# Optimization experiments

Measured on AMD Instinct MI355X. Metric: run time of the kernel, lower is better.

## Reference

```python
import jax, jax.numpy as jnp
import numpy as np

NUM_HEADS = 2
D = 512
D_HID = 2048


def _layer_norm(x, g, b, eps):
    mu = jnp.mean(x, axis=-1, keepdims=True)
    var = jnp.var(x, axis=-1, keepdims=True)
    return (x - mu) * jax.lax.rsqrt(var + eps) * g + b


def _attn_block(Q, K, V, resnet, Wq, Wk, Wv, ln_g, ln_b, w1, w2, fln_g, fln_b):
    # Linear projections (torch Linear: x @ W.T), no bias
    q = Q @ Wq.T
    k = K @ Wk.T
    v = V @ Wv.T
    B, N, C = q.shape
    gs = C // NUM_HEADS  # group size per head
    # split channels into heads == reshape [B,N,H,gs] -> [B,H,N,gs]
    qh = q.reshape(B, N, NUM_HEADS, gs).transpose(0, 2, 1, 3)
    kh = k.reshape(B, K.shape[1], NUM_HEADS, gs).transpose(0, 2, 1, 3)
    vh = v.reshape(B, V.shape[1], NUM_HEADS, gs).transpose(0, 2, 1, 3)
    scores = jnp.einsum('bhqd,bhkd->bhqk', qh, kh) / jnp.sqrt(jnp.asarray(gs, q.dtype))
    attn = jax.nn.softmax(scores, axis=-1)
    out = jnp.einsum('bhqk,bhkd->bhqd', attn, vh)
    # concat heads back to channel dim
    out = out.transpose(0, 2, 1, 3).reshape(B, N, C)
    x = out + resnet
    x = _layer_norm(x, ln_g, ln_b, 1e-5)
    # FFN (dropout is identity in eval mode)
    residual = x
    y = jax.nn.relu(x @ w1.T) @ w2.T
    y = y + residual
    y = _layer_norm(y, fln_g, fln_b, 1e-6)
    return y


def setup_inputs() -> dict:
    key = jax.random.key(0)
    ks = jax.random.split(key, 16)
    B, N = 4, 2048
    Fm = jax.random.normal(ks[0], (B, N, D), dtype=jnp.float32)
    Fs = jax.random.normal(ks[1], (B, N, D), dtype=jnp.float32)
    Fq = jax.random.normal(ks[2], (B, N, D), dtype=jnp.float32)
    s = 0.02
    Wq = jax.random.normal(ks[3], (3, D, D), dtype=jnp.float32) * s
    Wk = jax.random.normal(ks[4], (3, D, D), dtype=jnp.float32) * s
    Wv = jax.random.normal(ks[5], (3, D, D), dtype=jnp.float32) * s
    ln_g = jnp.ones((3, D), dtype=jnp.float32)
    ln_b = jnp.zeros((3, D), dtype=jnp.float32)
    w1 = jax.random.normal(ks[6], (3, D_HID, D), dtype=jnp.float32) * s
    w2 = jax.random.normal(ks[7], (3, D, D_HID), dtype=jnp.float32) * s
    fln_g = jnp.ones((3, D), dtype=jnp.float32)
    fln_b = jnp.zeros((3, D), dtype=jnp.float32)
    return {"Fm": Fm, "Fs": Fs, "Fq": Fq, "Wq": Wq, "Wk": Wk, "Wv": Wv,
            "ln_g": ln_g, "ln_b": ln_b, "w1": w1, "w2": w2,
            "fln_g": fln_g, "fln_b": fln_b, "out_dim": 512}


def reference(Fm, Fs, Fq, Wq, Wk, Wv, ln_g, ln_b, w1, w2, fln_g, fln_b, out_dim):
    def blk(i, Q, K, V, resnet):
        return _attn_block(Q, K, V, resnet, Wq[i], Wk[i], Wv[i], ln_g[i], ln_b[i],
                           w1[i], w2[i], fln_g[i], fln_b[i])
    css = blk(0, Fs, Fs, Fm, Fm)
    cqq = blk(1, Fq, Fq, Fq, Fq)
    csq = blk(2, cqq, Fs, css, css)
    return csq
```

## Files before the change

### kernel.cpp

```cpp
#include <hip/hip_runtime.h>

typedef __bf16 bf16_t;
typedef __bf16 bf16x8 __attribute__((ext_vector_type(8)));
typedef __bf16 bf16x4 __attribute__((ext_vector_type(4)));
typedef float  f32x4  __attribute__((ext_vector_type(4)));

#define GAS __attribute__((address_space(1)))
#define LAS __attribute__((address_space(3)))

enum { EPI_BF16 = 0, EPI_RELU = 1 };

struct GPtrs {
    const bf16_t* A[6];
    const bf16_t* B[6];
    bf16_t*       C[6];
};

__global__ void probe_dtype(const unsigned* __restrict__ lng_bits, int* __restrict__ flag)
{
    *flag = (lng_bits[0] == 0x3F800000u) ? 0 : 1;
}

__global__ __launch_bounds__(256) void conv_any3(
    const void* __restrict__ s0, const void* __restrict__ s1, const void* __restrict__ s2,
    bf16_t* __restrict__ d0, bf16_t* __restrict__ d1, bf16_t* __restrict__ d2,
    const int* __restrict__ flag, int n8)
{
    int i = blockIdx.x * 256 + threadIdx.x;
    if (i >= n8) return;
    const void* src = (blockIdx.z == 0) ? s0 : (blockIdx.z == 1) ? s1 : s2;
    bf16_t*    dst = (blockIdx.z == 0) ? d0 : (blockIdx.z == 1) ? d1 : d2;
    if (*flag == 0) {
        const float4* s = (const float4*)src;
        float4 a = s[i * 2], b = s[i * 2 + 1];
        bf16x8 o = { (bf16_t)a.x, (bf16_t)a.y, (bf16_t)a.z, (bf16_t)a.w,
                     (bf16_t)b.x, (bf16_t)b.y, (bf16_t)b.z, (bf16_t)b.w };
        ((bf16x8*)dst)[i] = o;
    } else {
        ((uint4*)dst)[i] = ((const uint4*)src)[i];
    }
}

__global__ __launch_bounds__(256) void widen_ln4(
    const void* __restrict__ a, const void* __restrict__ b,
    const void* __restrict__ c, const void* __restrict__ d,
    float* __restrict__ dst, const int* __restrict__ flag, int n)
{
    int i = blockIdx.x * 256 + threadIdx.x;
    int seg = i / n, j = i - seg * n;
    if (seg >= 4) return;
    const void* s = (seg == 0) ? a : (seg == 1) ? b : (seg == 2) ? c : d;
    dst[i] = (*flag == 0) ? ((const float*)s)[j]
                          : (float)((const bf16_t*)s)[j];
}

template<int EPI, int TMv, int TNv, bool TABLE, int ZH, bool VT>
__global__ __launch_bounds__(256) void gemm_bt(
    GPtrs P, int K, int lda, int ldb, int ldc,
    long sAb, long sAh, long sBb, long sBh, long sCb, long sCh,
    float scale)
{
    constexpr int MF = TMv / 32, NF = TNv / 32;
    constexpr int STG = 2 * (TMv + TNv) * 32;
    constexpr int RPK = TMv * TNv;
    constexpr int SME = (STG > RPK) ? STG : RPK;
    __shared__ __align__(16) bf16_t smem[SME];
    bf16_t* Asb = smem;
    bf16_t* Bsb = smem + 2 * TMv * 32;

    const int z = blockIdx.z;
    const bf16_t* A; const bf16_t* B; bf16_t* C; long cOff = 0;
    if constexpr (TABLE) {
        A = P.A[z]; B = P.B[z]; C = P.C[z];
    } else {
        const int half = z / ZH, zz = z % ZH;
        const long zb = zz >> 1, zh = zz & 1;
        A = P.A[half] + zb * sAb + zh * sAh;
        B = P.B[half] + zb * sBb + zh * sBh;
        C = P.C[half]; cOff = zb * sCb + zh * sCh;
    }

    int m_t, n_t;
    {
        const int gx = gridDim.x, gy = gridDim.y;
        if ((gy & 7) == 0) {
            const int L = blockIdx.y * gx + blockIdx.x;
            const int band_h = gy >> 3;
            const int r = L >> 3;
            m_t = (L & 7) * band_h + (r % band_h);
            n_t = r / band_h;
        } else { m_t = blockIdx.y; n_t = blockIdx.x; }
    }
    const int n0 = n_t * TNv;
    const int m0 = m_t * TMv;

    const int tid  = threadIdx.x;
    const int wave = tid >> 6, lane = tid & 63;
    const int wm = (wave >> 1) * (TMv / 2);
    const int wn = (wave & 1) * (TNv / 2);
    const int lrow = lane & 15, lquad = lane >> 4;
    const int rq   = (lquad ^ ((lrow >> 1) & 3)) * 8;
    const int drow = lane >> 2;
    const int dcol = (((lane & 3) ^ ((lane >> 3) & 3))) * 8;

    f32x4 acc[MF][NF];
    #pragma unroll
    for (int i = 0; i < MF; i++)
        #pragma unroll
        for (int j = 0; j < NF; j++) acc[i][j] = (f32x4){0.f, 0.f, 0.f, 0.f};

    const bf16_t* aP = A + (long)(m0 + wave * (TMv / 4) + drow) * lda + dcol;
    const bf16_t* bP = B + (long)(n0 + wave * (TNv / 4) + drow) * ldb + dcol;
    bf16_t* asW = Asb + wave * (TMv / 4) * 32;
    bf16_t* bsW = Bsb + wave * (TNv / 4) * 32;

    for (int kk = 0; kk < K; kk += 64) {
        __syncthreads();
        #pragma unroll
        for (int p = 0; p < 2; p++) {
            #pragma unroll
            for (int i = 0; i < TMv / 64; i++)
                __builtin_amdgcn_global_load_lds(
                    (GAS void*)(aP + p * 32 + (long)i * 16 * lda),
                    (LAS void*)(asW + p * TMv * 32 + i * 16 * 32), 16, 0, 0);
            #pragma unroll
            for (int i = 0; i < TNv / 64; i++)
                __builtin_amdgcn_global_load_lds(
                    (GAS void*)(bP + p * 32 + (long)i * 16 * ldb),
                    (LAS void*)(bsW + p * TNv * 32 + i * 16 * 32), 16, 0, 0);
        }
        aP += 64; bP += 64;
        __syncthreads();

        #pragma unroll
        for (int p = 0; p < 2; p++) {
            bf16x8 af[MF], bfr[NF];
            #pragma unroll
            for (int mi = 0; mi < MF; mi++)
                af[mi] = *(const bf16x8*)&Asb[(p * TMv + wm + mi * 16 + lrow) * 32 + rq];
            #pragma unroll
            for (int ni = 0; ni < NF; ni++)
                bfr[ni] = *(const bf16x8*)&Bsb[(p * TNv + wn + ni * 16 + lrow) * 32 + rq];
            #pragma unroll
            for (int mi = 0; mi < MF; mi++)
                #pragma unroll
                for (int ni = 0; ni < NF; ni++)
                    acc[mi][ni] = __builtin_amdgcn_mfma_f32_16x16x32_bf16(
                        af[mi], bfr[ni], acc[mi][ni], 0, 0, 0);
        }
    }

    if (VT && (z % 3 == 2)) {
        #pragma unroll
        for (int mi = 0; mi < MF; mi++)
            #pragma unroll
            for (int ni = 0; ni < NF; ni++) {
                const int mr = m0 + wm + mi * 16 + lquad * 4;
                const int nc = n0 + wn + ni * 16 + lrow;
                const int b = mr >> 11, s = mr & 2047;
                const int h = nc >> 8,  d = nc & 255;
                bf16x4 t = { (bf16_t)(acc[mi][ni][0]),
                             (bf16_t)(acc[mi][ni][1]),
                             (bf16_t)(acc[mi][ni][2]),
                             (bf16_t)(acc[mi][ni][3]) };
                *(bf16x4*)&C[(((long)(b * 2 + h) * 256 + d) << 11) + s] = t;
            }
        return;
    }

    __syncthreads();
    #pragma unroll
    for (int mi = 0; mi < MF; mi++)
        #pragma unroll
        for (int ni = 0; ni < NF; ni++)
            #pragma unroll
            for (int r = 0; r < 4; r++) {
                float v = acc[mi][ni][r] * scale;
                if (EPI == EPI_RELU) v = fmaxf(v, 0.f);
                smem[(wm + mi * 16 + lquad * 4 + r) * TNv + wn + ni * 16 + lrow] = (bf16_t)v;
            }
    __syncthreads();
    constexpr int TPR = TNv / 8;
    constexpr int RPP = 256 / TPR;
    const int srow = tid / TPR;
    const int scol = (tid % TPR) * 8;
    #pragma unroll
    for (int pass = 0; pass < TMv / RPP; pass++) {
        const int rr = pass * RPP + srow;
        bf16x8 vv = *(const bf16x8*)&smem[rr * TNv + scol];
        *(bf16x8*)&C[cOff + (long)(m0 + rr) * ldc + n0 + scol] = vv;
    }
}

__global__ __launch_bounds__(256) void softmax_rows(bf16_t* __restrict__ buf)
{
    const long base = (long)blockIdx.x * 2048;
    const int tid = threadIdx.x;
    const int wave = tid >> 6, lane = tid & 63;
    __shared__ float red[8];
    bf16x8 x = *(const bf16x8*)&buf[base + tid * 8];
    float v[8];
    float mx = -1e30f;
    #pragma unroll
    for (int j = 0; j < 8; j++) { v[j] = (float)x[j]; mx = fmaxf(mx, v[j]); }
    for (int off = 32; off; off >>= 1) mx = fmaxf(mx, __shfl_xor(mx, off));
    if (lane == 0) red[wave] = mx;
    __syncthreads();
    mx = fmaxf(fmaxf(red[0], red[1]), fmaxf(red[2], red[3]));
    float s = 0.f;
    #pragma unroll
    for (int j = 0; j < 8; j++) { v[j] = __expf(v[j] - mx); s += v[j]; }
    for (int off = 32; off; off >>= 1) s += __shfl_xor(s, off);
    if (lane == 0) red[4 + wave] = s;
    __syncthreads();
    s = red[4] + red[5] + red[6] + red[7];
    const float inv = 1.f / s;
    bf16x8 y;
    #pragma unroll
    for (int j = 0; j < 8; j++) y[j] = (bf16_t)(v[j] * inv);
    *(bf16x8*)&buf[base + tid * 8] = y;
}

__global__ __launch_bounds__(256) void add_ln2(
    const bf16_t* xA, const bf16_t* rA, const float* gA, const float* bA, bf16_t* oA,
    const bf16_t* xB, const bf16_t* rB, const float* gB, const float* bB, bf16_t* oB,
    float eps, int splitRows)
{
    const int wave = threadIdx.x >> 6, lane = threadIdx.x & 63;
    long row = (long)blockIdx.x * 4 + wave;
    const bf16_t* xin; const bf16_t* res; const float* g; const float* bias; bf16_t* out;
    if (row >= splitRows) {
        row -= splitRows;
        xin = xB; res = rB; g = gB; bias = bB; out = oB;
    } else {
        xin = xA; res = rA; g = gA; bias = bA; out = oA;
    }
    const long base = row * 512 + lane * 8;
    bf16x8 a8 = *(const bf16x8*)&xin[base];
    bf16x8 r8 = *(const bf16x8*)&res[base];
    float v[8];
    #pragma unroll
    for (int j = 0; j < 8; j++) v[j] = (float)a8[j] + (float)r8[j];
    float s = 0.f, s2 = 0.f;
    #pragma unroll
    for (int j = 0; j < 8; j++) { s += v[j]; s2 += v[j] * v[j]; }
    for (int off = 32; off; off >>= 1) { s += __shfl_xor(s, off); s2 += __shfl_xor(s2, off); }
    const float mu  = s * (1.f / 512.f);
    const float var = s2 * (1.f / 512.f) - mu * mu;
    const float rs  = rsqrtf(var + eps);
    const int c0 = lane * 8;
    float4 g0 = *(const float4*)&g[c0];
    float4 g1 = *(const float4*)&g[c0 + 4];
    float4 b0 = *(const float4*)&bias[c0];
    float4 b1 = *(const float4*)&bias[c0 + 4];
    float gv[8] = { g0.x, g0.y, g0.z, g0.w, g1.x, g1.y, g1.z, g1.w };
    float bv[8] = { b0.x, b0.y, b0.z, b0.w, b1.x, b1.y, b1.z, b1.w };
    #pragma unroll
    for (int j = 0; j < 8; j++)
        out[base + j] = (bf16_t)((v[j] - mu) * rs * gv[j] + bv[j]);
}

__global__ __launch_bounds__(256) void add_ln_f32(
    const bf16_t* xin, const bf16_t* __restrict__ res,
    const float* __restrict__ g, const float* __restrict__ bias,
    float* out, float eps)
{
    const int wave = threadIdx.x >> 6, lane = threadIdx.x & 63;
    const long row = (long)blockIdx.x * 4 + wave;
    const long base = row * 512 + lane * 8;
    bf16x8 a8 = *(const bf16x8*)&xin[base];
    bf16x8 r8 = *(const bf16x8*)&res[base];
    float v[8];
    #pragma unroll
    for (int j = 0; j < 8; j++) v[j] = (float)a8[j] + (float)r8[j];
    float s = 0.f, s2 = 0.f;
    #pragma unroll
    for (int j = 0; j < 8; j++) { s += v[j]; s2 += v[j] * v[j]; }
    for (int off = 32; off; off >>= 1) { s += __shfl_xor(s, off); s2 += __shfl_xor(s2, off); }
    const float mu  = s * (1.f / 512.f);
    const float var = s2 * (1.f / 512.f) - mu * mu;
    const float rs  = rsqrtf(var + eps);
    const int c0 = lane * 8;
    float4 g0 = *(const float4*)&g[c0];
    float4 g1 = *(const float4*)&g[c0 + 4];
    float4 b0 = *(const float4*)&bias[c0];
    float4 b1 = *(const float4*)&bias[c0 + 4];
    float gv[8] = { g0.x, g0.y, g0.z, g0.w, g1.x, g1.y, g1.z, g1.w };
    float bv[8] = { b0.x, b0.y, b0.z, b0.w, b1.x, b1.y, b1.z, b1.w };
    #pragma unroll
    for (int j = 0; j < 8; j++)
        out[base + j] = (v[j] - mu) * rs * gv[j] + bv[j];
}

extern "C" void kernel_launch(void* const* d_in, const int* in_sizes, int n_in,
                              void* d_out, int out_size, void* d_ws, size_t ws_size,
                              hipStream_t stream)
{
    const void* Fm    = d_in[0];
    const void* Fs    = d_in[1];
    const void* Fq    = d_in[2];
    const void* Wq    = d_in[3];
    const void* Wk    = d_in[4];
    const void* Wv    = d_in[5];
    const void* ln_g  = d_in[6];
    const void* ln_b  = d_in[7];
    const void* w1    = d_in[8];
    const void* w2    = d_in[9];
    const void* fln_g = d_in[10];
    const void* fln_b = d_in[11];
    (void)in_sizes; (void)n_in; (void)out_size; (void)ws_size;

    char* ws = (char*)d_ws;
    size_t off = 0;
    auto take = [&](size_t bytes) {
        char* p = ws + off;
        off += (bytes + 255) & ~(size_t)255;
        return p;
    };
    const size_t NT = 8192ul * 512;

    int*    flag = (int*)take(256);
    float*  lnw  = (float*)take(4ul * 1536 * 4);
    bf16_t* Fm_b = (bf16_t*)take(NT * 2);
    bf16_t* Fs_b = (bf16_t*)take(NT * 2);
    bf16_t* Fq_b = (bf16_t*)take(NT * 2);
    bf16_t* wqb  = (bf16_t*)take(3ul * 512 * 512 * 2);
    bf16_t* wkb  = (bf16_t*)take(3ul * 512 * 512 * 2);
    bf16_t* wvb  = (bf16_t*)take(3ul * 512 * 512 * 2);
    bf16_t* w1b  = (bf16_t*)take(3ul * 2048 * 512 * 2);
    bf16_t* w2b  = (bf16_t*)take(3ul * 512 * 2048 * 2);
    bf16_t* q0   = (bf16_t*)take(NT * 2);
    bf16_t* k0   = (bf16_t*)take(NT * 2);
    bf16_t* q1   = (bf16_t*)take(NT * 2);
    bf16_t* k1   = (bf16_t*)take(NT * 2);
    bf16_t* vT0  = (bf16_t*)take(NT * 2);
    bf16_t* vT1  = (bf16_t*)take(NT * 2);
    bf16_t* scb  = (bf16_t*)take(2ul * 8 * 2048 * 2048 * 2);

    bf16_t* sc0 = scb;
    bf16_t* sc1 = scb + 8ul * 2048 * 2048;
    bf16_t* ao0 = q0;  bf16_t* ao1 = q1;
    bf16_t* x0  = k0;  bf16_t* x1  = k1;
    bf16_t* h0  = scb; bf16_t* h1  = scb + 16ul * 1024 * 1024;
    bf16_t* y0  = vT0; bf16_t* y1  = vT1;
    bf16_t* css = Fm_b;
    bf16_t* cqq = Fq_b;
    bf16_t* q2  = q0;  bf16_t* k2  = k0;  bf16_t* vT2 = vT0;
    bf16_t* sc2 = scb; bf16_t* ao2 = q1;  bf16_t* x2  = k1;
    bf16_t* h2  = scb + 32ul * 1024 * 1024;  bf16_t* y2 = vT1;

    dim3 blk(256);
    probe_dtype<<<dim3(1), dim3(1), 0, stream>>>((const unsigned*)ln_g, flag);

    conv_any3<<<dim3(2048, 1, 3), blk, 0, stream>>>(
        Fm, Fs, Fq, Fm_b, Fs_b, Fq_b, flag, (int)(NT / 8));
    conv_any3<<<dim3(384, 1, 3), blk, 0, stream>>>(
        Wq, Wk, Wv, wqb, wkb, wvb, flag, (int)(3ul * 512 * 512 / 8));
    conv_any3<<<dim3(1536, 1, 2), blk, 0, stream>>>(
        w1, w2, w2, w1b, w2b, w2b, flag, (int)(3ul * 2048 * 512 / 8));
    widen_ln4<<<dim3(24), blk, 0, stream>>>(ln_g, ln_b, fln_g, fln_b, lnw, flag, 1536);

    auto W  = [&](bf16_t* base, int i, size_t n) { return (const bf16_t*)(base + (size_t)i * n); };
    const float* g1[3]; const float* b1[3]; const float* g2[3]; const float* b2[3];
    for (int i = 0; i < 3; i++) {
        g1[i] = lnw + i * 512;            b1[i] = lnw + 1536 + i * 512;
        g2[i] = lnw + 2 * 1536 + i * 512; b2[i] = lnw + 3 * 1536 + i * 512;
    }

    {
        GPtrs P{};
        P.A[0] = Fs_b; P.A[1] = Fs_b; P.A[2] = Fm_b;
        P.A[3] = Fq_b; P.A[4] = Fq_b; P.A[5] = Fq_b;
        P.B[0] = W(wqb, 0, 512*512); P.B[1] = W(wkb, 0, 512*512); P.B[2] = W(wvb, 0, 512*512);
        P.B[3] = W(wqb, 1, 512*512); P.B[4] = W(wkb, 1, 512*512); P.B[5] = W(wvb, 1, 512*512);
        P.C[0] = q0; P.C[1] = k0; P.C[2] = vT0;
        P.C[3] = q1; P.C[4] = k1; P.C[5] = vT1;
        gemm_bt<EPI_BF16, 128, 64, true, 1, true><<<dim3(8, 64, 6), blk, 0, stream>>>(
            P, 512, 512, 512, 512, 0, 0, 0, 0, 0, 0, 1.f);
    }
    {
        GPtrs P{}; P.A[0] = q0; P.A[1] = q1; P.B[0] = k0; P.B[1] = k1;
        P.C[0] = sc0; P.C[1] = sc1;
        gemm_bt<EPI_BF16, 128, 128, false, 8, false><<<dim3(16, 16, 16), blk, 0, stream>>>(
            P, 256, 512, 512, 2048,
            1048576L, 256L, 1048576L, 256L, 8388608L, 4194304L, 0.0625f);
    }
    softmax_rows<<<dim3(32768), blk, 0, stream>>>(scb);
    {
        GPtrs P{}; P.A[0] = sc0; P.A[1] = sc1; P.B[0] = vT0; P.B[1] = vT1;
        P.C[0] = ao0; P.C[1] = ao1;
        gemm_bt<EPI_BF16, 128, 64, false, 8, false><<<dim3(4, 16, 16), blk, 0, stream>>>(
            P, 2048, 2048, 2048, 512,
            8388608L, 4194304L, 1048576L, 524288L, 1048576L, 256L, 1.f);
    }
    add_ln2<<<dim3(4096), blk, 0, stream>>>(
        ao0, Fm_b, g1[0], b1[0], x0,
        ao1, Fq_b, g1[1], b1[1], x1, 1e-5f, 8192);
    {
        GPtrs P{}; P.A[0] = x0; P.A[1] = x1;
        P.B[0] = W(w1b, 0, 2048*512); P.B[1] = W(w1b, 1, 2048*512);
        P.C[0] = h0; P.C[1] = h1;
        gemm_bt<EPI_RELU, 128, 128, false, 1, false><<<dim3(16, 64, 2), blk, 0, stream>>>(
            P, 512, 512, 512, 2048, 0, 0, 0, 0, 0, 0, 1.f);
    }
    {
        GPtrs P{}; P.A[0] = h0; P.A[1] = h1;
        P.B[0] = W(w2b, 0, 512*2048); P.B[1] = W(w2b, 1, 512*2048);
        P.C[0] = y0; P.C[1] = y1;
        gemm_bt<EPI_BF16, 128, 64, false, 1, false><<<dim3(8, 64, 2), blk, 0, stream>>>(
            P, 2048, 2048, 2048, 512, 0, 0, 0, 0, 0, 0, 1.f);
    }
    add_ln2<<<dim3(4096), blk, 0, stream>>>(
        y0, x0, g2[0], b2[0], css,
        y1, x1, g2[1], b2[1], cqq, 1e-6f, 8192);

    {
        GPtrs P{};
        P.A[0] = cqq; P.A[1] = Fs_b; P.A[2] = css;
        P.B[0] = W(wqb, 2, 512*512); P.B[1] = W(wkb, 2, 512*512); P.B[2] = W(wvb, 2, 512*512);
        P.C[0] = q2; P.C[1] = k2; P.C[2] = vT2;
        gemm_bt<EPI_BF16, 128, 64, true, 1, true><<<dim3(8, 64, 3), blk, 0, stream>>>(
            P, 512, 512, 512, 512, 0, 0, 0, 0, 0, 0, 1.f);
    }
    {
        GPtrs P{}; P.A[0] = q2; P.B[0] = k2; P.C[0] = sc2;
        gemm_bt<EPI_BF16, 128, 128, false, 8, false><<<dim3(16, 16, 8), blk, 0, stream>>>(
            P, 256, 512, 512, 2048,
            1048576L, 256L, 1048576L, 256L, 8388608L, 4194304L, 0.0625f);
    }
    softmax_rows<<<dim3(16384), blk, 0, stream>>>(sc2);
    {
        GPtrs P{}; P.A[0] = sc2; P.B[0] = vT2; P.C[0] = ao2;
        gemm_bt<EPI_BF16, 128, 64, false, 8, false><<<dim3(4, 16, 8), blk, 0, stream>>>(
            P, 2048, 2048, 2048, 512,
            8388608L, 4194304L, 1048576L, 524288L, 1048576L, 256L, 1.f);
    }
    add_ln2<<<dim3(2048), blk, 0, stream>>>(
        ao2, css, g1[2], b1[2], x2,
        ao2, css, g1[2], b1[2], x2, 1e-5f, 1 << 30);
    {
        GPtrs P{}; P.A[0] = x2; P.B[0] = W(w1b, 2, 2048*512); P.C[0] = h2;
        gemm_bt<EPI_RELU, 128, 128, false, 1, false><<<dim3(16, 64, 1), blk, 0, stream>>>(
            P, 512, 512, 512, 2048, 0, 0, 0, 0, 0, 0, 1.f);
    }
    {
        GPtrs P{}; P.A[0] = h2; P.B[0] = W(w2b, 2, 512*2048); P.C[0] = y2;
        gemm_bt<EPI_BF16, 128, 64, false, 1, false><<<dim3(8, 64, 1), blk, 0, stream>>>(
            P, 2048, 2048, 2048, 512, 0, 0, 0, 0, 0, 0, 1.f);
    }
    add_ln_f32<<<dim3(2048), blk, 0, stream>>>(
        y2, x2, g2[2], b2[2], (float*)d_out, 1e-6f);
}
```

Before: 624.6 us.

## Generalize GEMM warp layout, use 128x128 tiles with 8-wave blocks for long-K GEMMs

The GEMM template gains warp-grid parameters (WM x WN waves), so block size and per-wave fragment counts vary, and the global-to-LDS load mapping is rewritten to spread rows across all threads. The QKV projections and the long-K GEMMs (attention PV, FFN down-projection) switch from 128x64 to 128x128 tiles, the long-K ones running 512-thread blocks with 2x4 waves. The epilogue LDS staging gains an XOR swizzle to reduce bank conflicts. Wider tiles halve redundant A-tile loads but give fewer blocks per launch and more LDS per block, which can lower occupancy.

```diff
diff --git a/kernel.cpp b/kernel.cpp
--- a/kernel.cpp
+++ b/kernel.cpp
@@ -54,13 +54,14 @@
                           : (float)((const bf16_t*)s)[j];
 }
 
-template<int EPI, int TMv, int TNv, bool TABLE, int ZH, bool VT>
-__global__ __launch_bounds__(256) void gemm_bt(
+template<int EPI, int TMv, int TNv, int WM, int WN, bool TABLE, int ZH, bool VT>
+__global__ __launch_bounds__(WM * WN * 64, (WM * WN == 8) ? 4 : 2) void gemm_bt(
     GPtrs P, int K, int lda, int ldb, int ldc,
     long sAb, long sAh, long sBb, long sBh, long sCb, long sCh,
     float scale)
 {
-    constexpr int MF = TMv / 32, NF = TNv / 32;
+    constexpr int THREADS = WM * WN * 64;
+    constexpr int MF = TMv / WM / 16, NF = TNv / WN / 16;
     constexpr int STG = 2 * (TMv + TNv) * 32;
     constexpr int RPK = TMv * TNv;
     constexpr int SME = (STG > RPK) ? STG : RPK;
@@ -96,12 +97,15 @@
 
     const int tid  = threadIdx.x;
     const int wave = tid >> 6, lane = tid & 63;
-    const int wm = (wave >> 1) * (TMv / 2);
-    const int wn = (wave & 1) * (TNv / 2);
+    const int wm = (wave / WN) * (TMv / WM);
+    const int wn = (wave % WN) * (TNv / WN);
     const int lrow = lane & 15, lquad = lane >> 4;
     const int rq   = (lquad ^ ((lrow >> 1) & 3)) * 8;
-    const int drow = lane >> 2;
-    const int dcol = (((lane & 3) ^ ((lane >> 3) & 3))) * 8;
+    const int srow0 = tid >> 2;
+    const int scol0 = ((tid & 3) ^ ((tid >> 3) & 3)) * 8;
+    constexpr int ITA = (TMv * 4) / THREADS;
+    constexpr int ITB = (TNv * 4) / THREADS;
+    constexpr int RSW = THREADS / 4;
 
     f32x4 acc[MF][NF];
     #pragma unroll
@@ -109,25 +113,24 @@
         #pragma unroll
         for (int j = 0; j < NF; j++) acc[i][j] = (f32x4){0.f, 0.f, 0.f, 0.f};
 
-    const bf16_t* aP = A + (long)(m0 + wave * (TMv / 4) + drow) * lda + dcol;
-    const bf16_t* bP = B + (long)(n0 + wave * (TNv / 4) + drow) * ldb + dcol;
-    bf16_t* asW = Asb + wave * (TMv / 4) * 32;
-    bf16_t* bsW = Bsb + wave * (TNv / 4) * 32;
+    const bf16_t* aP = A + (long)(m0 + srow0) * lda + scol0;
+    const bf16_t* bP = B + (long)(n0 + srow0) * ldb + scol0;
+    const int wbase = wave * 64 * 8;
 
     for (int kk = 0; kk < K; kk += 64) {
         __syncthreads();
         #pragma unroll
         for (int p = 0; p < 2; p++) {
             #pragma unroll
-            for (int i = 0; i < TMv / 64; i++)
+            for (int i = 0; i < ITA; i++)
                 __builtin_amdgcn_global_load_lds(
-                    (GAS void*)(aP + p * 32 + (long)i * 16 * lda),
-                    (LAS void*)(asW + p * TMv * 32 + i * 16 * 32), 16, 0, 0);
-            #pragma unroll
-            for (int i = 0; i < TNv / 64; i++)
+                    (GAS void*)(aP + p * 32 + (long)i * RSW * lda),
+                    (LAS void*)(Asb + p * TMv * 32 + i * THREADS * 8 + wbase), 16, 0, 0);
+            #pragma unroll
+            for (int i = 0; i < ITB; i++)
                 __builtin_amdgcn_global_load_lds(
-                    (GAS void*)(bP + p * 32 + (long)i * 16 * ldb),
-                    (LAS void*)(bsW + p * TNv * 32 + i * 16 * 32), 16, 0, 0);
+                    (GAS void*)(bP + p * 32 + (long)i * RSW * ldb),
+                    (LAS void*)(Bsb + p * TNv * 32 + i * THREADS * 8 + wbase), 16, 0, 0);
         }
         aP += 64; bP += 64;
         __syncthreads();
@@ -177,17 +180,21 @@
             for (int r = 0; r < 4; r++) {
                 float v = acc[mi][ni][r] * scale;
                 if (EPI == EPI_RELU) v = fmaxf(v, 0.f);
-                smem[(wm + mi * 16 + lquad * 4 + r) * TNv + wn + ni * 16 + lrow] = (bf16_t)v;
+                const int rI = wm + mi * 16 + lquad * 4 + r;
+                const int c  = wn + ni * 16 + lrow;
+                const int cs = c ^ (((((rI >> 2) & 3) ^ (rI & 3))) << 4);
+                smem[rI * TNv + cs] = (bf16_t)v;
             }
     __syncthreads();
     constexpr int TPR = TNv / 8;
-    constexpr int RPP = 256 / TPR;
+    constexpr int RPP = THREADS / TPR;
     const int srow = tid / TPR;
     const int scol = (tid % TPR) * 8;
     #pragma unroll
     for (int pass = 0; pass < TMv / RPP; pass++) {
         const int rr = pass * RPP + srow;
-        bf16x8 vv = *(const bf16x8*)&smem[rr * TNv + scol];
+        const int cc = scol ^ (((((rr >> 2) & 3) ^ (rr & 3))) << 4);
+        bf16x8 vv = *(const bf16x8*)&smem[rr * TNv + cc];
         *(bf16x8*)&C[cOff + (long)(m0 + rr) * ldc + n0 + scol] = vv;
     }
 }
@@ -349,7 +356,7 @@
     bf16_t* sc2 = scb; bf16_t* ao2 = q1;  bf16_t* x2  = k1;
     bf16_t* h2  = scb + 32ul * 1024 * 1024;  bf16_t* y2 = vT1;
 
-    dim3 blk(256);
+    dim3 blk(256), blk8(512);
     probe_dtype<<<dim3(1), dim3(1), 0, stream>>>((const unsigned*)ln_g, flag);
 
     conv_any3<<<dim3(2048, 1, 3), blk, 0, stream>>>(
@@ -375,13 +382,13 @@
         P.B[3] = W(wqb, 1, 512*512); P.B[4] = W(wkb, 1, 512*512); P.B[5] = W(wvb, 1, 512*512);
         P.C[0] = q0; P.C[1] = k0; P.C[2] = vT0;
         P.C[3] = q1; P.C[4] = k1; P.C[5] = vT1;
-        gemm_bt<EPI_BF16, 128, 64, true, 1, true><<<dim3(8, 64, 6), blk, 0, stream>>>(
+        gemm_bt<EPI_BF16, 128, 128, 2, 2, true, 1, true><<<dim3(4, 64, 6), blk, 0, stream>>>(
             P, 512, 512, 512, 512, 0, 0, 0, 0, 0, 0, 1.f);
     }
     {
         GPtrs P{}; P.A[0] = q0; P.A[1] = q1; P.B[0] = k0; P.B[1] = k1;
         P.C[0] = sc0; P.C[1] = sc1;
-        gemm_bt<EPI_BF16, 128, 128, false, 8, false><<<dim3(16, 16, 16), blk, 0, stream>>>(
+        gemm_bt<EPI_BF16, 128, 128, 2, 2, false, 8, false><<<dim3(16, 16, 16), blk, 0, stream>>>(
             P, 256, 512, 512, 2048,
             1048576L, 256L, 1048576L, 256L, 8388608L, 4194304L, 0.0625f);
     }
@@ -389,7 +396,7 @@
     {
         GPtrs P{}; P.A[0] = sc0; P.A[1] = sc1; P.B[0] = vT0; P.B[1] = vT1;
         P.C[0] = ao0; P.C[1] = ao1;
-        gemm_bt<EPI_BF16, 128, 64, false, 8, false><<<dim3(4, 16, 16), blk, 0, stream>>>(
+        gemm_bt<EPI_BF16, 128, 128, 2, 4, false, 8, false><<<dim3(2, 16, 16), blk8, 0, stream>>>(
             P, 2048, 2048, 2048, 512,
             8388608L, 4194304L, 1048576L, 524288L, 1048576L, 256L, 1.f);
     }
@@ -400,14 +407,14 @@
         GPtrs P{}; P.A[0] = x0; P.A[1] = x1;
         P.B[0] = W(w1b, 0, 2048*512); P.B[1] = W(w1b, 1, 2048*512);
         P.C[0] = h0; P.C[1] = h1;
-        gemm_bt<EPI_RELU, 128, 128, false, 1, false><<<dim3(16, 64, 2), blk, 0, stream>>>(
+        gemm_bt<EPI_RELU, 128, 128, 2, 2, false, 1, false><<<dim3(16, 64, 2), blk, 0, stream>>>(
             P, 512, 512, 512, 2048, 0, 0, 0, 0, 0, 0, 1.f);
     }
     {
         GPtrs P{}; P.A[0] = h0; P.A[1] = h1;
         P.B[0] = W(w2b, 0, 512*2048); P.B[1] = W(w2b, 1, 512*2048);
         P.C[0] = y0; P.C[1] = y1;
-        gemm_bt<EPI_BF16, 128, 64, false, 1, false><<<dim3(8, 64, 2), blk, 0, stream>>>(
+        gemm_bt<EPI_BF16, 128, 128, 2, 4, false, 1, false><<<dim3(4, 64, 2), blk8, 0, stream>>>(
             P, 2048, 2048, 2048, 512, 0, 0, 0, 0, 0, 0, 1.f);
     }
     add_ln2<<<dim3(4096), blk, 0, stream>>>(
@@ -419,19 +426,19 @@
         P.A[0] = cqq; P.A[1] = Fs_b; P.A[2] = css;
         P.B[0] = W(wqb, 2, 512*512); P.B[1] = W(wkb, 2, 512*512); P.B[2] = W(wvb, 2, 512*512);
         P.C[0] = q2; P.C[1] = k2; P.C[2] = vT2;
-        gemm_bt<EPI_BF16, 128, 64, true, 1, true><<<dim3(8, 64, 3), blk, 0, stream>>>(
+        gemm_bt<EPI_BF16, 128, 128, 2, 2, true, 1, true><<<dim3(4, 64, 3), blk, 0, stream>>>(
             P, 512, 512, 512, 512, 0, 0, 0, 0, 0, 0, 1.f);
     }
     {
         GPtrs P{}; P.A[0] = q2; P.B[0] = k2; P.C[0] = sc2;
-        gemm_bt<EPI_BF16, 128, 128, false, 8, false><<<dim3(16, 16, 8), blk, 0, stream>>>(
+        gemm_bt<EPI_BF16, 128, 128, 2, 2, false, 8, false><<<dim3(16, 16, 8), blk, 0, stream>>>(
             P, 256, 512, 512, 2048,
             1048576L, 256L, 1048576L, 256L, 8388608L, 4194304L, 0.0625f);
     }
     softmax_rows<<<dim3(16384), blk, 0, stream>>>(sc2);
     {
         GPtrs P{}; P.A[0] = sc2; P.B[0] = vT2; P.C[0] = ao2;
-        gemm_bt<EPI_BF16, 128, 64, false, 8, false><<<dim3(4, 16, 8), blk, 0, stream>>>(
+        gemm_bt<EPI_BF16, 128, 128, 2, 4, false, 8, false><<<dim3(2, 16, 8), blk8, 0, stream>>>(
             P, 2048, 2048, 2048, 512,
             8388608L, 4194304L, 1048576L, 524288L, 1048576L, 256L, 1.f);
     }
@@ -440,12 +447,12 @@
         ao2, css, g1[2], b1[2], x2, 1e-5f, 1 << 30);
     {
         GPtrs P{}; P.A[0] = x2; P.B[0] = W(w1b, 2, 2048*512); P.C[0] = h2;
-        gemm_bt<EPI_RELU, 128, 128, false, 1, false><<<dim3(16, 64, 1), blk, 0, stream>>>(
+        gemm_bt<EPI_RELU, 128, 128, 2, 2, false, 1, false><<<dim3(16, 64, 1), blk, 0, stream>>>(
             P, 512, 512, 512, 2048, 0, 0, 0, 0, 0, 0, 1.f);
     }
     {
         GPtrs P{}; P.A[0] = h2; P.B[0] = W(w2b, 2, 512*2048); P.C[0] = y2;
-        gemm_bt<EPI_BF16, 128, 64, false, 1, false><<<dim3(8, 64, 1), blk, 0, stream>>>(
+        gemm_bt<EPI_BF16, 128, 128, 2, 4, false, 1, false><<<dim3(4, 64, 1), blk8, 0, stream>>>(
             P, 2048, 2048, 2048, 512, 0, 0, 0, 0, 0, 0, 1.f);
     }
     add_ln_f32<<<dim3(2048), blk, 0, stream>>>(
```

New measurement: 585.9 us. -6.2%, faster.
